# Kernel optimization log

Hardware: AMD Instinct MI355X
Metric: run time of the kernel (lower is better)

The kernel has to match this reference:

```python
import jax, jax.numpy as jnp
import numpy as np
from jax import lax


def setup_inputs() -> dict:
    key = jax.random.key(0)
    k1, k2, k3, k4, k5 = jax.random.split(key, 5)
    b, c_in, c_out, h, wdim, k = 16, 256, 256, 64, 64, 3
    return {
        "x": jax.random.normal(k1, (b, c_in, h, wdim), dtype=jnp.float32),
        "w_style": jax.random.normal(k2, (b, 512), dtype=jnp.float32),
        "W": jax.random.normal(k3, (c_out, c_in, k, k), dtype=jnp.float32),
        "aff_w": jax.random.normal(k4, (c_in, 512), dtype=jnp.float32) * 0.02,
        "aff_b": jax.random.normal(k5, (c_in,), dtype=jnp.float32) * 0.02,
    }


def reference(x, w_style, W, aff_w, aff_b):
    # x: [b, c_in, h, w]; w_style: [b, 512]; W: [c_out, c_in, k, k]
    k = W.shape[-1]
    pad = k // 2
    # style modulation: s = affine(w) + 1, per-sample per-input-channel scale
    s = w_style @ aff_w.T + aff_b + 1.0                     # [b, c_in]
    wgt = W[None] * s[:, None, :, None, None]               # [b, c_out, c_in, k, k]
    # demodulation: normalize each per-sample output filter
    d = lax.rsqrt(jnp.sum(wgt * wgt, axis=(2, 3, 4)) + 1e-8)  # [b, c_out]
    wgt = wgt * d[:, :, None, None, None]
    # per-sample conv (math-equivalent to the groups=b grouped-conv trick)
    def conv_one(xi, wi):
        # xi: [c_in, h, w], wi: [c_out, c_in, k, k]
        return lax.conv_general_dilated(
            xi[None], wi,
            window_strides=(1, 1),
            padding=[(pad, pad), (pad, pad)],
            dimension_numbers=("NCHW", "OIHW", "NCHW"),
        )[0]
    return jax.vmap(conv_one)(x, wgt)                       # [b, c_out, h, w]
```

## Files before the change

### kernel.cpp

```cpp
#include <hip/hip_runtime.h>
#include <hip/hip_bf16.h>

#define BATCH 16
#define CIN   256
#define COUT  256
#define HH    64
#define WW    64
#define SDIM  512
#define NPIX  4096
#define PADH  66
#define PADW  66

typedef __hip_bfloat16 bf16;
typedef __attribute__((ext_vector_type(8))) short short8;
typedef __attribute__((ext_vector_type(4))) float f32x4;

__device__ __forceinline__ void glds16(const void* g, void* l) {
    __builtin_amdgcn_global_load_lds(
        (const __attribute__((address_space(1))) unsigned int*)g,
        (__attribute__((address_space(3))) unsigned int*)l, 16, 0, 0);
}

__device__ __forceinline__ unsigned pkbf2(float a, float b) {
    __hip_bfloat162 h;
    h.x = __float2bfloat16(a);
    h.y = __float2bfloat16(b);
    unsigned u;
    __builtin_memcpy(&u, &h, 4);
    return u;
}

#define BAR()   __builtin_amdgcn_s_barrier()
#define VM0()   asm volatile("s_waitcnt vmcnt(0)" ::: "memory")

__global__ __launch_bounds__(256) void style_kernel(
    const float* __restrict__ w_style, const float* __restrict__ aff_w,
    const float* __restrict__ aff_b, float* __restrict__ s)
{
    const int b = blockIdx.x, c = threadIdx.x;
    __shared__ float ws[SDIM];
    for (int j = c; j < SDIM; j += 256) ws[j] = w_style[b * SDIM + j];
    __syncthreads();
    const float* aw = aff_w + (size_t)c * SDIM;
    float acc = 0.f;
#pragma unroll 4
    for (int j = 0; j < SDIM; j += 4) {
        const float4 a = *(const float4*)(aw + j);
        acc += a.x * ws[j] + a.y * ws[j + 1] + a.z * ws[j + 2] + a.w * ws[j + 3];
    }
    s[b * CIN + c] = acc + aff_b[c] + 1.0f;
}

__global__ __launch_bounds__(256) void prep_kernel(
    const float* __restrict__ W, const float* __restrict__ s,
    const float* __restrict__ x,
    bf16* __restrict__ wt, bf16* __restrict__ xt)
{
    __shared__ union {
        float    wl[CIN * 9];
        bf16     t[WW][CIN + 2];
        unsigned t32[WW][(CIN + 2) / 2];
    } sh;
    const int tid = threadIdx.x;

    if (blockIdx.x < BATCH * COUT) {
        const int bc = blockIdx.x, b = bc >> 8, co = bc & 255, ci = tid;
        const float* wrow = W + (size_t)co * (CIN * 9);
        for (int i = ci; i < CIN * 9 / 4; i += 256)
            *(float4*)&sh.wl[i * 4] = *(const float4*)(wrow + i * 4);
        __syncthreads();
        const float sv = s[b * CIN + ci];
        float m[9], part = 0.f;
#pragma unroll
        for (int r = 0; r < 9; ++r) { m[r] = sh.wl[ci * 9 + r] * sv; part += m[r] * m[r]; }
#pragma unroll
        for (int off = 32; off > 0; off >>= 1)
            part += __shfl_down(part, off, 64);
        __shared__ float red[4];
        if ((ci & 63) == 0) red[ci >> 6] = part;
        __syncthreads();
        const float d = rsqrtf(red[0] + red[1] + red[2] + red[3] + 1e-8f);
#pragma unroll
        for (int r = 0; r < 9; ++r)
            wt[(((size_t)b * 9 + r) * COUT + co) * CIN + ci] = __float2bfloat16(m[r] * d);
    } else {
        const int xb  = blockIdx.x - BATCH * COUT;
        const int row = xb % PADH, b = xb / PADH;
        bf16* orow = xt + (((size_t)b * PADH + row) * PADW) * CIN;

        if (row == 0 || row == PADH - 1) {
            const uint4 z = {0, 0, 0, 0};
            for (int i = tid; i < PADW * CIN / 8; i += 256) ((uint4*)orow)[i] = z;
            return;
        }
        const float* xr = x + ((size_t)b * CIN * NPIX) + (size_t)(row - 1) * WW;
        for (int i = tid; i < (CIN / 2) * (WW / 4); i += 256) {
            const int ci = (i >> 4) * 2, c4 = (i & 15) * 4;
            const float4 v0 = *(const float4*)(xr + (size_t)ci * NPIX + c4);
            const float4 v1 = *(const float4*)(xr + (size_t)(ci + 1) * NPIX + c4);
            sh.t32[c4 + 0][ci >> 1] = pkbf2(v0.x, v1.x);
            sh.t32[c4 + 1][ci >> 1] = pkbf2(v0.y, v1.y);
            sh.t32[c4 + 2][ci >> 1] = pkbf2(v0.z, v1.z);
            sh.t32[c4 + 3][ci >> 1] = pkbf2(v0.w, v1.w);
        }
        __syncthreads();
        for (int i = tid; i < PADW * (CIN / 8); i += 256) {
            const int col = i >> 5, c8 = (i & 31) * 8;
            uint4 v = {0, 0, 0, 0};
            if (col > 0 && col < PADW - 1) {
                const unsigned* tp = (const unsigned*)&sh.t[col - 1][c8];
                v.x = tp[0]; v.y = tp[1]; v.z = tp[2]; v.w = tp[3];
            }
            ((uint4*)orow)[i] = v;
        }
    }
}

__global__ __launch_bounds__(512, 2) void gemm_kernel(
    const bf16* __restrict__ xt,
    const bf16* __restrict__ wt,
    float* __restrict__ out)
{
    const int bid = blockIdx.x;
    const int b  = bid & 15;
    const int nt = bid >> 4;
    const int tid  = threadIdx.x;
    const int wave = tid >> 6, lane = tid & 63;
    const int wm = wave >> 2, wn = wave & 3;
    const int lm = lane & 15, quad = lane >> 4;

    __shared__ bf16 Ash[2][256 * 64];
    __shared__ bf16 Bsh[6 * PADW * 64];

    f32x4 acc[8][4] = {};

    const bf16* xb = xt + (size_t)b * PADH * PADW * CIN;
    const bf16* wb = wt + (size_t)b * 9 * COUT * CIN;

    int p0[4];
#pragma unroll
    for (int ni = 0; ni < 4; ++ni)
        p0[ni] = (1 + wn) * PADW + ni * 16 + lm + 1;

    auto stageA = [&](int r, int c, int buf) {
        const bf16* wr = wb + (size_t)r * (COUT * CIN) + c * 64;
#pragma unroll
        for (int k = 0; k < 4; ++k) {
            const int i = tid + k * 512;
            const int co = i >> 3, pc = i & 7;
            const int lc = pc ^ (co & 7);
            glds16(wr + co * CIN + lc * 8, Ash[buf] + i * 8);
        }
    };
    auto stageB = [&](int c) {
        const int ci0 = c * 64;
        for (int i = tid; i < 6 * PADW * 8; i += 512) {
            const int row = i / (PADW * 8);
            const int j   = i - row * (PADW * 8);
            const int col = j >> 3, pc = j & 7;
            const int p   = row * PADW + col;
            const int lc  = pc ^ (p & 7);
            glds16(xb + (((size_t)(nt * 4 + row) * PADW + col) * CIN + ci0 + lc * 8),
                   Bsh + i * 8);
        }
    };
    auto readA = [&](short8* af, int kk, int mih, int buf) {
#pragma unroll
        for (int mi = 0; mi < 4; ++mi) {
            const int arow = wm * 128 + (mih * 4 + mi) * 16 + lm;
            const int lc   = kk * 4 + quad;
            af[mi] = *(const short8*)(Ash[buf] + arow * 64 + (lc ^ (arow & 7)) * 8);
        }
    };
    auto readB = [&](short8* bfr, int kk, int dpx) {
#pragma unroll
        for (int ni = 0; ni < 4; ++ni) {
            const int p  = p0[ni] + dpx;
            const int lc = kk * 4 + quad;
            bfr[ni] = *(const short8*)(Bsh + p * 64 + (lc ^ (p & 7)) * 8);
        }
    };
    auto mfma16 = [&](int half, const short8* af, const short8* bfr) {
        __builtin_amdgcn_s_setprio(1);
#pragma unroll
        for (int mi = 0; mi < 4; ++mi)
#pragma unroll
            for (int ni = 0; ni < 4; ++ni)
                acc[half * 4 + mi][ni] = __builtin_amdgcn_mfma_f32_16x16x32_bf16(
                    af[mi], bfr[ni], acc[half * 4 + mi][ni], 0, 0, 0);
        __builtin_amdgcn_s_setprio(0);
    };

    stageB(0);
    stageA(0, 0, 0);
    __syncthreads();

    short8 afE[4], afO[4], bfE[4], bfO[4];
    readA(afE, 0, 0, 0);
    readB(bfE, 0, -PADW - 1);

    int cur = 0;
#pragma unroll 1
    for (int c = 0; c < 4; ++c) {
#pragma unroll 1
        for (int r = 0; r < 9; ++r) {
            const bool last = (c == 3) && (r == 8);
            const int nr = (r == 8) ? 0 : r + 1;
            const int dpx  = (r / 3 - 1) * PADW + (r % 3 - 1);
            const int dpxn = (nr / 3 - 1) * PADW + (nr % 3 - 1);

            readA(afO, 0, 1, cur);
            if (!last) stageA(nr, (r == 8) ? c + 1 : c, cur ^ 1);
            BAR();
            mfma16(0, afE, bfE);
            BAR();

            readA(afE, 1, 0, cur);
            readB(bfO, 1, dpx);
            BAR();
            mfma16(1, afO, bfE);
            BAR();

            if (r == 8 && c < 3) {
                __syncthreads();
                stageB(c + 1);
            }
            readA(afO, 1, 1, cur);
            BAR();
            mfma16(0, afE, bfO);
            BAR();

            if (!last) VM0();
            BAR();
            if (!last) {
                readA(afE, 0, 0, cur ^ 1);
                readB(bfE, 0, dpxn);
            }
            mfma16(1, afO, bfO);
            BAR();
            cur ^= 1;
        }
    }

    float* ob = out + (size_t)b * COUT * NPIX + nt * 256;
#pragma unroll
    for (int mi = 0; mi < 8; ++mi) {
        const int cl = wm * 128 + mi * 16 + quad * 4;
#pragma unroll
        for (int ni = 0; ni < 4; ++ni) {
            const int px = wn * 64 + ni * 16 + lm;
#pragma unroll
            for (int v = 0; v < 4; ++v)
                ob[(size_t)(cl + v) * NPIX + px] = acc[mi][ni][v];
        }
    }
}

template <bool FUSE_S>
__global__ __launch_bounds__(256) void conv_mod_kernel(
    const float* __restrict__ x, const float* __restrict__ W,
    const float* __restrict__ s_pre, const float* __restrict__ w_style,
    const float* __restrict__ aff_w, const float* __restrict__ aff_b,
    float* __restrict__ out)
{
    const int bc = blockIdx.x, b = bc >> 8, co = bc & 255, tid = threadIdx.x;
    __shared__ float wsh[CIN * 9];
    __shared__ float red[CIN];
    float sv;
    if (FUSE_S) {
        __shared__ float wst[SDIM];
        for (int j = tid; j < SDIM; j += 256) wst[j] = w_style[b * SDIM + j];
        __syncthreads();
        const float* aw = aff_w + tid * SDIM;
        float a2 = 0.f;
#pragma unroll 8
        for (int j = 0; j < SDIM; ++j) a2 += wst[j] * aw[j];
        sv = a2 + aff_b[tid] + 1.0f;
    } else sv = s_pre[b * CIN + tid];
    {
        const float* wp = W + (co * CIN + tid) * 9;
        float m[9], part = 0.f;
#pragma unroll
        for (int r = 0; r < 9; ++r) { m[r] = wp[r] * sv; part += m[r] * m[r]; }
        red[tid] = part;
        __syncthreads();
#pragma unroll
        for (int off = CIN / 2; off > 0; off >>= 1) {
            if (tid < off) red[tid] += red[tid + off];
            __syncthreads();
        }
        const float d = rsqrtf(red[0] + 1e-8f);
#pragma unroll
        for (int r = 0; r < 9; ++r) wsh[tid * 9 + r] = m[r] * d;
        __syncthreads();
    }
    const int p = blockIdx.y * 256 + tid, y = p >> 6, xx = p & 63;
    const bool vt = y > 0, vb = y < HH - 1, vl = xx > 0, vr = xx < WW - 1;
    const bool val[9] = { vt && vl, vt, vt && vr, vl, true, vr, vb && vl, vb, vb && vr };
    const int off9[9] = { -WW - 1, -WW, -WW + 1, -1, 0, 1, WW - 1, WW, WW + 1 };
    const float* xbp = x + (size_t)b * CIN * NPIX + p;
    float acc = 0.f;
    for (int ci = 0; ci < CIN; ++ci) {
        const float* xp = xbp + ci * NPIX;
        const float* wp = wsh + ci * 9;
#pragma unroll
        for (int r = 0; r < 9; ++r) acc += (val[r] ? xp[off9[r]] : 0.f) * wp[r];
    }
    out[(size_t)bc * NPIX + p] = acc;
}

extern "C" void kernel_launch(void* const* d_in, const int* in_sizes, int n_in,
                              void* d_out, int out_size, void* d_ws, size_t ws_size,
                              hipStream_t stream) {
    const float* x       = (const float*)d_in[0];
    const float* w_style = (const float*)d_in[1];
    const float* W       = (const float*)d_in[2];
    const float* aff_w   = (const float*)d_in[3];
    const float* aff_b   = (const float*)d_in[4];
    float* out = (float*)d_out;

    const size_t wt_off  = 65536;
    const size_t wt_sz   = (size_t)BATCH * 9 * COUT * CIN * sizeof(bf16);
    const size_t xt_off  = wt_off + wt_sz;
    const size_t xt_sz   = (size_t)BATCH * PADH * PADW * CIN * sizeof(bf16);
    const size_t need    = xt_off + xt_sz;

    if (ws_size >= need) {
        float* s  = (float*)d_ws;
        bf16* wt  = (bf16*)((char*)d_ws + wt_off);
        bf16* xt  = (bf16*)((char*)d_ws + xt_off);
        style_kernel<<<dim3(BATCH), dim3(256), 0, stream>>>(w_style, aff_w, aff_b, s);
        prep_kernel<<<dim3(BATCH * COUT + BATCH * PADH), dim3(256), 0, stream>>>(
            W, s, x, wt, xt);
        gemm_kernel<<<dim3(BATCH * 16), dim3(512), 0, stream>>>(xt, wt, out);
    } else if (ws_size >= (size_t)(BATCH * CIN * sizeof(float))) {
        float* s = (float*)d_ws;
        style_kernel<<<dim3(BATCH), dim3(256), 0, stream>>>(w_style, aff_w, aff_b, s);
        conv_mod_kernel<false><<<dim3(BATCH * COUT, NPIX / 256), dim3(256), 0, stream>>>(
            x, W, s, w_style, aff_w, aff_b, out);
    } else {
        conv_mod_kernel<true><<<dim3(BATCH * COUT, NPIX / 256), dim3(256), 0, stream>>>(
            x, W, nullptr, w_style, aff_w, aff_b, out);
    }
}
```

Baseline: 215.0 us.

## Shrink GEMM tiles to 128x128 with 256-thread blocks for more workgroups

Splits each implicit-GEMM block from a 256-channel by 256-pixel tile (8 waves) into a 128-channel by 128-pixel tile (4 waves), giving 1024 workgroups instead of 256. It also shrinks the LDS A and B buffers and the accumulator count per wave. The aim is to fill all CUs of the MI355X, since 256 blocks is about one per CU, and to allow more resident blocks per CU. The cost is lower data reuse: each block restages more weight and input halo data per output.

Result: slower. 223.3 us (+3.9%).

```diff
diff --git a/kernel.cpp b/kernel.cpp
--- a/kernel.cpp
+++ b/kernel.cpp
@@ -116,37 +116,41 @@
     }
 }
 
-__global__ __launch_bounds__(512, 2) void gemm_kernel(
+__global__ __launch_bounds__(256, 2) void gemm_kernel(
     const bf16* __restrict__ xt,
     const bf16* __restrict__ wt,
     float* __restrict__ out)
 {
     const int bid = blockIdx.x;
     const int b  = bid & 15;
-    const int nt = bid >> 4;
+    const int mt = (bid >> 4) & 1;
+    const int nt = bid >> 5;
     const int tid  = threadIdx.x;
     const int wave = tid >> 6, lane = tid & 63;
-    const int wm = wave >> 2, wn = wave & 3;
+    const int wm = wave >> 1, wn = wave & 1;
     const int lm = lane & 15, quad = lane >> 4;
 
-    __shared__ bf16 Ash[2][256 * 64];
-    __shared__ bf16 Bsh[6 * PADW * 64];
-
-    f32x4 acc[8][4] = {};
-
+    __shared__ bf16 Ash[2][128 * 64];
+    __shared__ bf16 Bsh[4 * PADW * 64];
+
+    f32x4 acc[4][4] = {};
+
+    const int y0 = nt * 2;
     const bf16* xb = xt + (size_t)b * PADH * PADW * CIN;
-    const bf16* wb = wt + (size_t)b * 9 * COUT * CIN;
+    const bf16* wb = wt + (size_t)b * 9 * COUT * CIN + (size_t)mt * 128 * CIN;
 
     int p0[4];
 #pragma unroll
-    for (int ni = 0; ni < 4; ++ni)
-        p0[ni] = (1 + wn) * PADW + ni * 16 + lm + 1;
+    for (int ni = 0; ni < 4; ++ni) {
+        const int px = wn * 64 + ni * 16 + lm;
+        p0[ni] = (1 + (px >> 6)) * PADW + (px & 63) + 1;
+    }
 
     auto stageA = [&](int r, int c, int buf) {
         const bf16* wr = wb + (size_t)r * (COUT * CIN) + c * 64;
 #pragma unroll
         for (int k = 0; k < 4; ++k) {
-            const int i = tid + k * 512;
+            const int i = tid + k * 256;
             const int co = i >> 3, pc = i & 7;
             const int lc = pc ^ (co & 7);
             glds16(wr + co * CIN + lc * 8, Ash[buf] + i * 8);
@@ -154,25 +158,25 @@
     };
     auto stageB = [&](int c) {
         const int ci0 = c * 64;
-        for (int i = tid; i < 6 * PADW * 8; i += 512) {
+        for (int i = tid; i < 4 * PADW * 8; i += 256) {
             const int row = i / (PADW * 8);
             const int j   = i - row * (PADW * 8);
             const int col = j >> 3, pc = j & 7;
             const int p   = row * PADW + col;
             const int lc  = pc ^ (p & 7);
-            glds16(xb + (((size_t)(nt * 4 + row) * PADW + col) * CIN + ci0 + lc * 8),
+            glds16(xb + (((size_t)(y0 + row) * PADW + col) * CIN + ci0 + lc * 8),
                    Bsh + i * 8);
         }
     };
-    auto readA = [&](short8* af, int kk, int mih, int buf) {
-#pragma unroll
-        for (int mi = 0; mi < 4; ++mi) {
-            const int arow = wm * 128 + (mih * 4 + mi) * 16 + lm;
+    auto readA2 = [&](short8* af, int kk, int mlo, int buf) {
+#pragma unroll
+        for (int mi = 0; mi < 2; ++mi) {
+            const int arow = wm * 64 + (mlo + mi) * 16 + lm;
             const int lc   = kk * 4 + quad;
             af[mi] = *(const short8*)(Ash[buf] + arow * 64 + (lc ^ (arow & 7)) * 8);
         }
     };
-    auto readB = [&](short8* bfr, int kk, int dpx) {
+    auto readB4 = [&](short8* bfr, int kk, int dpx) {
 #pragma unroll
         for (int ni = 0; ni < 4; ++ni) {
             const int p  = p0[ni] + dpx;
@@ -180,14 +184,14 @@
             bfr[ni] = *(const short8*)(Bsh + p * 64 + (lc ^ (p & 7)) * 8);
         }
     };
-    auto mfma16 = [&](int half, const short8* af, const short8* bfr) {
+    auto mfma8 = [&](int mlo, const short8* af, const short8* bfr) {
         __builtin_amdgcn_s_setprio(1);
 #pragma unroll
-        for (int mi = 0; mi < 4; ++mi)
+        for (int mi = 0; mi < 2; ++mi)
 #pragma unroll
             for (int ni = 0; ni < 4; ++ni)
-                acc[half * 4 + mi][ni] = __builtin_amdgcn_mfma_f32_16x16x32_bf16(
-                    af[mi], bfr[ni], acc[half * 4 + mi][ni], 0, 0, 0);
+                acc[mlo + mi][ni] = __builtin_amdgcn_mfma_f32_16x16x32_bf16(
+                    af[mi], bfr[ni], acc[mlo + mi][ni], 0, 0, 0);
         __builtin_amdgcn_s_setprio(0);
     };
 
@@ -195,9 +199,9 @@
     stageA(0, 0, 0);
     __syncthreads();
 
-    short8 afE[4], afO[4], bfE[4], bfO[4];
-    readA(afE, 0, 0, 0);
-    readB(bfE, 0, -PADW - 1);
+    short8 afE[2], afO[2], bfE[4], bfO[4];
+    readA2(afE, 0, 0, 0);
+    readB4(bfE, 0, -PADW - 1);
 
     int cur = 0;
 #pragma unroll 1
@@ -209,43 +213,43 @@
             const int dpx  = (r / 3 - 1) * PADW + (r % 3 - 1);
             const int dpxn = (nr / 3 - 1) * PADW + (nr % 3 - 1);
 
-            readA(afO, 0, 1, cur);
+            readA2(afO, 0, 2, cur);
             if (!last) stageA(nr, (r == 8) ? c + 1 : c, cur ^ 1);
             BAR();
-            mfma16(0, afE, bfE);
-            BAR();
-
-            readA(afE, 1, 0, cur);
-            readB(bfO, 1, dpx);
-            BAR();
-            mfma16(1, afO, bfE);
+            mfma8(0, afE, bfE);
+            BAR();
+
+            readA2(afE, 1, 0, cur);
+            readB4(bfO, 1, dpx);
+            BAR();
+            mfma8(2, afO, bfE);
             BAR();
 
             if (r == 8 && c < 3) {
                 __syncthreads();
                 stageB(c + 1);
             }
-            readA(afO, 1, 1, cur);
-            BAR();
-            mfma16(0, afE, bfO);
+            readA2(afO, 1, 2, cur);
+            BAR();
+            mfma8(0, afE, bfO);
             BAR();
 
             if (!last) VM0();
             BAR();
             if (!last) {
-                readA(afE, 0, 0, cur ^ 1);
-                readB(bfE, 0, dpxn);
+                readA2(afE, 0, 0, cur ^ 1);
+                readB4(bfE, 0, dpxn);
             }
-            mfma16(1, afO, bfO);
+            mfma8(2, afO, bfO);
             BAR();
             cur ^= 1;
         }
     }
 
-    float* ob = out + (size_t)b * COUT * NPIX + nt * 256;
-#pragma unroll
-    for (int mi = 0; mi < 8; ++mi) {
-        const int cl = wm * 128 + mi * 16 + quad * 4;
+    float* ob = out + (size_t)b * COUT * NPIX + (size_t)mt * 128 * NPIX + nt * 128;
+#pragma unroll
+    for (int mi = 0; mi < 4; ++mi) {
+        const int cl = wm * 64 + mi * 16 + quad * 4;
 #pragma unroll
         for (int ni = 0; ni < 4; ++ni) {
             const int px = wn * 64 + ni * 16 + lm;
@@ -332,7 +336,7 @@
         style_kernel<<<dim3(BATCH), dim3(256), 0, stream>>>(w_style, aff_w, aff_b, s);
         prep_kernel<<<dim3(BATCH * COUT + BATCH * PADH), dim3(256), 0, stream>>>(
             W, s, x, wt, xt);
-        gemm_kernel<<<dim3(BATCH * 16), dim3(512), 0, stream>>>(xt, wt, out);
+        gemm_kernel<<<dim3(BATCH * 64), dim3(256), 0, stream>>>(xt, wt, out);
     } else if (ws_size >= (size_t)(BATCH * CIN * sizeof(float))) {
         float* s = (float*)d_ws;
         style_kernel<<<dim3(BATCH), dim3(256), 0, stream>>>(w_style, aff_w, aff_b, s);
```
